# Optimization experiments

Hardware: AMD Instinct MI355X
Metric: run time of the kernel (lower is better)

## Reference

```python
import jax, jax.numpy as jnp
import numpy as np

N = 50000
E = 800000
NODE_F = 5
MAP_F = 32
EDGE_F = 4
HID = 64
RNN = 20
RNN_E = 8
LAT = 32
OUT = 4


def setup_inputs() -> dict:
    key = jax.random.key(0)
    ks = iter(jax.random.split(key, 40))
    def rn(shape, scale=0.1):
        return jax.random.normal(next(ks), shape, dtype=jnp.float32) * scale
    inp = {
        "x": rn((N, NODE_F), 1.0),
        "u": rn((N, MAP_F), 1.0),
        "edge_index": jax.random.randint(next(ks), (2, E), 0, N, dtype=jnp.int32),
        "edge_attr": rn((E, EDGE_F), 1.0),
        "h_node_h": rn((N, RNN), 1.0),
        "h_node_c": rn((N, RNN), 1.0),
        "h_edge_h": rn((N, RNN_E), 1.0),
        "h_edge_c": rn((N, RNN_E), 1.0),
        # node-history LSTM (input = node_features + map_encoding_size = 37)
        "W_ih_n": rn((4 * RNN, NODE_F + MAP_F)), "W_hh_n": rn((4 * RNN, RNN)),
        "b_ih_n": jnp.zeros((4 * RNN,), jnp.float32), "b_hh_n": jnp.zeros((4 * RNN,), jnp.float32),
        # edge-history LSTM (input = latent_edge_features)
        "W_ih_e": rn((4 * RNN_E, LAT)), "W_hh_e": rn((4 * RNN_E, RNN_E)),
        "b_ih_e": jnp.zeros((4 * RNN_E,), jnp.float32), "b_hh_e": jnp.zeros((4 * RNN_E,), jnp.float32),
        # message edge MLP: in = 2*37 + 4 = 78 -> 64 -> 32
        "We1": rn((2 * (NODE_F + MAP_F) + EDGE_F, HID)), "be1": jnp.zeros((HID,), jnp.float32),
        "We2": rn((HID, LAT)), "be2": jnp.zeros((LAT,), jnp.float32),
        # GN_out edge MLP: in = 2*(rnn_size + rnn_edge_size) + 4 = 60 -> 64 -> 32
        "Wo1": rn((2 * (RNN + RNN_E) + EDGE_F, HID)), "bo1": jnp.zeros((HID,), jnp.float32),
        "Wo2": rn((HID, LAT)), "bo2": jnp.zeros((LAT,), jnp.float32),
        # GN_out node MLP: in = (rnn_size + rnn_edge_size) + latent = 60 -> 64 -> 4
        "Wn1": rn((RNN + RNN_E + LAT, HID)), "bn1": jnp.zeros((HID,), jnp.float32),
        "Wn2": rn((HID, OUT)), "bn2": jnp.zeros((OUT,), jnp.float32),
    }
    return inp


def _lstm_step(xin, h, c, Wih, Whh, bih, bhh):
    # torch gate order: i, f, g, o
    g = xin @ Wih.T + h @ Whh.T + bih + bhh
    i, f, gg, o = jnp.split(g, 4, axis=-1)
    c_new = jax.nn.sigmoid(f) * c + jax.nn.sigmoid(i) * jnp.tanh(gg)
    h_new = jax.nn.sigmoid(o) * jnp.tanh(c_new)
    return h_new, c_new


def _segment_mean(vals, idx, n):
    s = jax.ops.segment_sum(vals, idx, num_segments=n)
    cnt = jax.ops.segment_sum(jnp.ones((vals.shape[0], 1), vals.dtype), idx, num_segments=n)
    return s / jnp.maximum(cnt, 1.0)


def _edge_mlp(src, dst, edge_attr, W1, b1, W2, b2):
    h = jnp.concatenate([src, dst, edge_attr], axis=-1)
    return jax.nn.relu(h @ W1 + b1) @ W2 + b2


def reference(x, u, edge_index, edge_attr, h_node_h, h_node_c, h_edge_h, h_edge_c,
              W_ih_n, W_hh_n, b_ih_n, b_hh_n, W_ih_e, W_hh_e, b_ih_e, b_hh_e,
              We1, be1, We2, be2, Wo1, bo1, Wo2, bo2, Wn1, bn1, Wn2, bn2):
    n = x.shape[0]
    xu = jnp.concatenate([x, u], axis=-1)  # [N, 37]
    # node history RNN step
    node_hist, node_c = _lstm_step(xu, h_node_h, h_node_c, W_ih_n, W_hh_n, b_ih_n, b_hh_n)
    # message GN: gather -> edge MLP
    row, col = edge_index[0], edge_index[1]
    messages = _edge_mlp(xu[row], xu[col], edge_attr, We1, be1, We2, be2)  # [E, 32]
    # edge history RNN: aggregate messages per receiving node, then LSTM step
    agg_msg = _segment_mean(messages, col, n)  # [N, 32]
    edge_hist, edge_c = _lstm_step(agg_msg, h_edge_h, h_edge_c, W_ih_e, W_hh_e, b_ih_e, b_hh_e)
    # output GN block
    full = jnp.concatenate([node_hist, edge_hist], axis=-1)  # [N, 28]
    e2 = _edge_mlp(full[row], full[col], edge_attr, Wo1, bo1, Wo2, bo2)  # [E, 32]
    agg2 = _segment_mean(e2, col, n)  # [N, 32]
    node_in = jnp.concatenate([full, agg2], axis=-1)  # [N, 60]
    out = jax.nn.relu(node_in @ Wn1 + bn1) @ Wn2 + bn2  # [N, 4]
    return (out, node_hist, node_c, edge_hist, edge_c)
```

## Files before the change

kernel.cpp:

```cpp
#include <hip/hip_runtime.h>
#include <math.h>

#define NN 50000
#define EE 800000
#define SBLK ((NN + 255) / 256)

typedef short bf16x8 __attribute__((ext_vector_type(8)));
typedef float f32x4 __attribute__((ext_vector_type(4)));
typedef unsigned short ushort_t;
#define MFMA16(a, b, c) __builtin_amdgcn_mfma_f32_16x16x32_bf16(a, b, c, 0, 0, 0)

__device__ __forceinline__ float sigmoidf_(float x) { return 1.0f / (1.0f + __expf(-x)); }

__device__ __forceinline__ unsigned short f2bf(float f) {
    unsigned u = __builtin_bit_cast(unsigned, f);
    u += 0x7FFFu + ((u >> 16) & 1u);
    return (unsigned short)(u >> 16);
}
__device__ __forceinline__ float bf2f(unsigned short v) {
    unsigned u = (unsigned)v << 16;
    return __builtin_bit_cast(float, u);
}
__device__ __forceinline__ unsigned pk2(float a, float b) {
    return ((unsigned)f2bf(b) << 16) | (unsigned)f2bf(a);
}

#define W1ST_A 104
#define W1ST_B 72
#define C1ST_  72
#define PW1A (64 * W1ST_A)
#define PW2A (32 * C1ST_)
#define PW1B (64 * W1ST_B)
#define PW2B (32 * C1ST_)

__global__ __launch_bounds__(256) void pack_w_k(
    const float* __restrict__ We1, const float* __restrict__ We2,
    const float* __restrict__ Wo1, const float* __restrict__ Wo2,
    ushort_t* __restrict__ pw)
{
    ushort_t* pw1a = pw;
    ushort_t* pw2a = pw1a + PW1A;
    ushort_t* pw1b = pw2a + PW2A;
    ushort_t* pw2b = pw1b + PW1B;
    int tid = threadIdx.x;

    for (int i = tid; i < PW1A; i += 256) {
        int n = i / W1ST_A, nk = i - n * W1ST_A;
        int kp = 0; bool z = false;
        if (nk < 37) kp = nk;
        else if (nk < 40) z = true;
        else if (nk < 77) kp = nk - 3;
        else if (nk < 80) z = true;
        else if (nk < 84) kp = nk - 6;
        else z = true;
        pw1a[i] = z ? (ushort_t)0 : f2bf(We1[kp * 64 + n]);
    }
    for (int i = tid; i < PW2A; i += 256) {
        int n = i / C1ST_, k = i - n * C1ST_;
        pw2a[i] = (k < 64) ? f2bf(We2[k * 32 + n]) : (ushort_t)0;
    }
    for (int i = tid; i < PW1B; i += 256) {
        int n = i / W1ST_B, nk = i - n * W1ST_B;
        int kp = 0; bool z = false;
        if (nk < 28) kp = nk;
        else if (nk < 32) z = true;
        else if (nk < 64) kp = nk - 4;
        else z = true;
        pw1b[i] = z ? (ushort_t)0 : f2bf(Wo1[kp * 64 + n]);
    }
    for (int i = tid; i < PW2B; i += 256) {
        int n = i / C1ST_, k = i - n * C1ST_;
        pw2b[i] = (k < 64) ? f2bf(Wo2[k * 32 + n]) : (ushort_t)0;
    }
}

__global__ __launch_bounds__(256) void node_lstm_k(
    const float* __restrict__ x, const float* __restrict__ u,
    const float* __restrict__ h0, const float* __restrict__ c0,
    const float* __restrict__ Wih, const float* __restrict__ Whh,
    const float* __restrict__ bih, const float* __restrict__ bhh,
    ushort_t* __restrict__ xu16, float* __restrict__ h_out, float* __restrict__ c_out)
{
    __shared__ float sWih[80 * 37];
    __shared__ float sWhh[80 * 20];
    __shared__ float sb[80];
    for (int i = threadIdx.x; i < 80 * 37; i += 256) sWih[i] = Wih[i];
    for (int i = threadIdx.x; i < 80 * 20; i += 256) sWhh[i] = Whh[i];
    if (threadIdx.x < 80) sb[threadIdx.x] = bih[threadIdx.x] + bhh[threadIdx.x];
    __syncthreads();
    int n = blockIdx.x * 256 + threadIdx.x;
    if (n >= NN) return;

    float xu[40];
#pragma unroll
    for (int k = 0; k < 5; k++) xu[k] = x[n * 5 + k];
#pragma unroll
    for (int k = 0; k < 32; k++) xu[5 + k] = u[n * 32 + k];
    xu[37] = 0.f; xu[38] = 0.f; xu[39] = 0.f;

    {
        unsigned w[20];
#pragma unroll
        for (int k = 0; k < 20; k++) w[k] = pk2(xu[2 * k], xu[2 * k + 1]);
        uint4* dst = (uint4*)(xu16 + (size_t)n * 40);
#pragma unroll
        for (int q = 0; q < 5; q++)
            dst[q] = make_uint4(w[q * 4], w[q * 4 + 1], w[q * 4 + 2], w[q * 4 + 3]);
    }

    float h[20];
#pragma unroll
    for (int k = 0; k < 20; k++) h[k] = h0[n * 20 + k];

#pragma unroll 1
    for (int r = 0; r < 20; r++) {
        float gi = sb[r], gf = sb[20 + r], gg = sb[40 + r], go = sb[60 + r];
#pragma unroll
        for (int k = 0; k < 37; k++) {
            float v = xu[k];
            gi = fmaf(v, sWih[r * 37 + k], gi);
            gf = fmaf(v, sWih[(20 + r) * 37 + k], gf);
            gg = fmaf(v, sWih[(40 + r) * 37 + k], gg);
            go = fmaf(v, sWih[(60 + r) * 37 + k], go);
        }
#pragma unroll
        for (int k = 0; k < 20; k++) {
            float v = h[k];
            gi = fmaf(v, sWhh[r * 20 + k], gi);
            gf = fmaf(v, sWhh[(20 + r) * 20 + k], gf);
            gg = fmaf(v, sWhh[(40 + r) * 20 + k], gg);
            go = fmaf(v, sWhh[(60 + r) * 20 + k], go);
        }
        float cr = c0[n * 20 + r];
        float cn = sigmoidf_(gf) * cr + sigmoidf_(gi) * tanhf(gg);
        float hn = sigmoidf_(go) * tanhf(cn);
        h_out[n * 20 + r] = hn;
        c_out[n * 20 + r] = cn;
    }
}

__global__ __launch_bounds__(256) void csr_count_k(const int* __restrict__ col,
                                                   int* __restrict__ count)
{
    int e = blockIdx.x * 256 + threadIdx.x;
    if (e < EE) atomicAdd(&count[col[e]], 1);
}

__global__ __launch_bounds__(256) void scan1_k(const int* __restrict__ count,
                                               int* __restrict__ bsum)
{
    __shared__ int red[256];
    int t = threadIdx.x;
    int i = blockIdx.x * 256 + t;
    red[t] = (i < NN) ? count[i] : 0;
    __syncthreads();
#pragma unroll
    for (int d = 128; d > 0; d >>= 1) {
        if (t < d) red[t] += red[t + d];
        __syncthreads();
    }
    if (t == 0) bsum[blockIdx.x] = red[0];
}

__global__ __launch_bounds__(256) void scan2_k(const int* __restrict__ bsum,
                                               int* __restrict__ bpre)
{
    __shared__ int s[256];
    int t = threadIdx.x;
    int v = (t < SBLK) ? bsum[t] : 0;
    s[t] = v;
    __syncthreads();
#pragma unroll
    for (int d = 1; d < 256; d <<= 1) {
        int w = (t >= d) ? s[t - d] : 0;
        __syncthreads();
        s[t] += w;
        __syncthreads();
    }
    if (t < SBLK) bpre[t] = s[t] - v;
}

__global__ __launch_bounds__(256) void scan3_k(const int* __restrict__ count,
                                               const int* __restrict__ bpre,
                                               int* __restrict__ offset,
                                               float* __restrict__ cntf)
{
    __shared__ int s[256];
    int t = threadIdx.x;
    int i = blockIdx.x * 256 + t;
    int v = (i < NN) ? count[i] : 0;
    s[t] = v;
    __syncthreads();
#pragma unroll
    for (int d = 1; d < 256; d <<= 1) {
        int w = (t >= d) ? s[t - d] : 0;
        __syncthreads();
        s[t] += w;
        __syncthreads();
    }
    if (i < NN) {
        offset[i] = bpre[blockIdx.x] + s[t] - v;
        cntf[i] = (float)v;
    }
}

__global__ __launch_bounds__(256) void csr_fill4_k(const int* __restrict__ row,
                                                   const int* __restrict__ col,
                                                   const float* __restrict__ eattr,
                                                   const int* __restrict__ offset,
                                                   int* __restrict__ cursor,
                                                   uint4* __restrict__ edat)
{
    int e = blockIdx.x * 256 + threadIdx.x;
    if (e >= EE) return;
    int c = col[e];
    int pos = atomicAdd(&cursor[c], 1);
    int slot = offset[c] + pos;
    float4 ev = *(const float4*)&eattr[(size_t)e * 4];
    edat[slot] = make_uint4((unsigned)row[e], (unsigned)c, pk2(ev.x, ev.y), pk2(ev.z, ev.w));
}

template <int F, int STRIDE, int INK>
__global__ __launch_bounds__(256, 5) void edge_mlp_fused_k(
    const ushort_t* __restrict__ feat,
    const uint4* __restrict__ edat,
    const int* __restrict__ offset, const int* __restrict__ count,
    const ushort_t* __restrict__ pw,
    const float* __restrict__ b1, const float* __restrict__ b2,
    float* __restrict__ agg)
{
    constexpr int S1 = INK / 32;
    constexpr int W1ST = INK + 8;
    constexpr int C1ST = C1ST_;
    constexpr int MST = 260;
    constexpr int ABYTES = (64 * W1ST + 32 * C1ST + 4 * 16 * C1ST) * 2;
    constexpr int BBYTES = 32 * MST * 2;
    constexpr int UBYTES = (ABYTES > BBYTES) ? ABYTES : BBYTES;
    constexpr int NU4 = (64 * W1ST + 32 * C1ST) / 8;

    __shared__ __align__(16) char ldsu[UBYTES];
    __shared__ int colLds[256];
    __shared__ unsigned char segStartA[256];
    __shared__ short segEndA[256];
    __shared__ int segCnt;

    ushort_t* sW1 = (ushort_t*)ldsu;
    ushort_t* sW2 = sW1 + 64 * W1ST;
    ushort_t* sC1 = sW2 + 32 * C1ST;
    ushort_t* msgT16 = (ushort_t*)ldsu;

    const int tid = threadIdx.x;
    const int B0 = blockIdx.x * 256;
    if (tid == 0) segCnt = 0;
    colLds[tid] = (int)edat[B0 + tid].y;

    {
        const uint4* src = (const uint4*)pw;
        uint4* dst = (uint4*)ldsu;
        for (int i = tid; i < NU4; i += 256) dst[i] = src[i];
    }
    __syncthreads();

    {
        bool isStart = (tid == 0) || (colLds[tid] != colLds[tid - 1]);
        if (isStart) {
            int node = colLds[tid];
            int off = offset[node], cn = count[node];
            int e = off + cn - B0; if (e > 256) e = 256;
            bool fullseg = (off >= B0) && (off + cn <= B0 + 256);
            int j = atomicAdd(&segCnt, 1);
            segStartA[j] = (unsigned char)tid;
            segEndA[j] = (short)(fullseg ? -e : e);
        }
    }

    const int wave = tid >> 6, lane = tid & 63;
    const int lr = lane & 15, jb = lane >> 4;
    const size_t slotBase = (size_t)B0 + (size_t)wave * 64;
    const float4* b1v = (const float4*)b1;
    ushort_t* myC1 = sC1 + wave * 16 * C1ST;
    const float bb2_0 = b2[lr], bb2_1 = b2[16 + lr];

    f32x4 acc2a[4][2];

#pragma unroll
    for (int q = 0; q < 4; q++) {
        bf16x8 xf[S1];
        {
            size_t slot = slotBase + (size_t)q * 16 + lr;
            uint4 ed = edat[slot];
            const ushort_t* xr = feat + (size_t)ed.x * STRIDE;
            const ushort_t* xc = feat + (size_t)ed.y * STRIDE;
            xf[0] = *(const bf16x8*)(xr + jb * 8);
            if (F == 37) {
                const ushort_t* p1 = (jb == 0) ? (xr + 32) : (xc + (jb - 1) * 8);
                xf[1] = *(const bf16x8*)p1;
                bf16x8 v;
                if (jb < 2) {
                    v = *(const bf16x8*)((jb == 0) ? (xc + 24) : (xc + 32));
                } else if (jb == 2) {
                    uint4 t = make_uint4(ed.z, ed.w, 0u, 0u);
                    v = __builtin_bit_cast(bf16x8, t);
                } else {
                    uint4 t = make_uint4(0u, 0u, 0u, 0u);
                    v = __builtin_bit_cast(bf16x8, t);
                }
                xf[2] = v;
            } else {
                if (jb < 3) {
                    xf[1] = *(const bf16x8*)(xc + jb * 8);
                } else {
                    uint2 lo = *(const uint2*)(xc + 24);
                    uint4 t = make_uint4(lo.x, lo.y, ed.z, ed.w);
                    xf[1] = __builtin_bit_cast(bf16x8, t);
                }
            }
        }

        f32x4 acc1[4];
#pragma unroll
        for (int mh = 0; mh < 4; mh++) {
            float4 bv = b1v[mh * 4 + jb];
            acc1[mh] = f32x4{bv.x, bv.y, bv.z, bv.w};
        }
#pragma unroll
        for (int s = 0; s < S1; s++) {
#pragma unroll
            for (int mh = 0; mh < 4; mh++) {
                bf16x8 wf = *(const bf16x8*)&sW1[(mh * 16 + lr) * W1ST + s * 32 + jb * 8];
                acc1[mh] = MFMA16(wf, xf[s], acc1[mh]);
            }
        }

#pragma unroll
        for (int mh = 0; mh < 4; mh++) {
            f32x4 a = acc1[mh];
            unsigned w0 = pk2(fmaxf(a[0], 0.f), fmaxf(a[1], 0.f));
            unsigned w1 = pk2(fmaxf(a[2], 0.f), fmaxf(a[3], 0.f));
            *(uint2*)&myC1[(jb * 4 + 0) * 0 + lr * C1ST + mh * 16 + jb * 4] = make_uint2(w0, w1);
        }

        acc2a[q][0] = f32x4{bb2_0, bb2_0, bb2_0, bb2_0};
        acc2a[q][1] = f32x4{bb2_1, bb2_1, bb2_1, bb2_1};
#pragma unroll
        for (int s2 = 0; s2 < 2; s2++) {
            bf16x8 w2f0 = *(const bf16x8*)&sW2[lr * C1ST + s2 * 32 + jb * 8];
            bf16x8 w2f1 = *(const bf16x8*)&sW2[(16 + lr) * C1ST + s2 * 32 + jb * 8];
            bf16x8 a2 = *(const bf16x8*)&myC1[lr * C1ST + s2 * 32 + jb * 8];
            acc2a[q][0] = MFMA16(a2, w2f0, acc2a[q][0]);
            acc2a[q][1] = MFMA16(a2, w2f1, acc2a[q][1]);
        }
    }

    __syncthreads();
#pragma unroll
    for (int q = 0; q < 4; q++) {
        int row = wave * 64 + q * 16 + jb * 4;
#pragma unroll
        for (int n = 0; n < 2; n++) {
            f32x4 a = acc2a[q][n];
            ushort_t* dst = &msgT16[(size_t)(n * 16 + lr) * MST + row];
            *(uint2*)dst = make_uint2(pk2(a[0], a[1]), pk2(a[2], a[3]));
        }
    }
    __syncthreads();

    {
        int f = lane & 31;
        int h = lane >> 5;
        const ushort_t* mrow = msgT16 + (size_t)f * MST;
        int nseg = segCnt;
        for (int j = wave; j < nseg; j += 4) {
            int s = segStartA[j];
            int ev = segEndA[j];
            bool fullseg = ev < 0;
            int e = fullseg ? -ev : ev;
            int node = colLds[s];
            float sum = 0.f;
            for (int i = s + h; i < e; i += 2) sum += bf2f(mrow[i]);
            sum += __shfl_xor(sum, 32);
            if (lane < 32) {
                float* dst = &agg[(size_t)node * 32 + f];
                if (fullseg) *dst = sum;
                else atomicAdd(dst, sum);
            }
        }
    }
}

__global__ __launch_bounds__(256) void edge_lstm_k(
    const float* __restrict__ agg, const float* __restrict__ cnt,
    const float* __restrict__ h0, const float* __restrict__ c0,
    const float* __restrict__ Wih, const float* __restrict__ Whh,
    const float* __restrict__ bih, const float* __restrict__ bhh,
    const float* __restrict__ node_h,
    float* __restrict__ h_out, float* __restrict__ c_out, ushort_t* __restrict__ full16)
{
    __shared__ float sWih[32 * 32];
    __shared__ float sWhh[32 * 8];
    __shared__ float sb[32];
    for (int i = threadIdx.x; i < 32 * 32; i += 256) sWih[i] = Wih[i];
    for (int i = threadIdx.x; i < 32 * 8; i += 256) sWhh[i] = Whh[i];
    if (threadIdx.x < 32) sb[threadIdx.x] = bih[threadIdx.x] + bhh[threadIdx.x];
    __syncthreads();
    int n = blockIdx.x * 256 + threadIdx.x;
    if (n >= NN) return;

    float inv = 1.0f / fmaxf(cnt[n], 1.0f);
    float msg[32];
#pragma unroll
    for (int k = 0; k < 32; k++) msg[k] = agg[(size_t)n * 32 + k] * inv;
    float h[8];
#pragma unroll
    for (int k = 0; k < 8; k++) h[k] = h0[n * 8 + k];

    float fl[32];
#pragma unroll
    for (int k = 0; k < 20; k++) fl[k] = node_h[n * 20 + k];
    fl[28] = 0.f; fl[29] = 0.f; fl[30] = 0.f; fl[31] = 0.f;

#pragma unroll
    for (int r = 0; r < 8; r++) {
        float gi = sb[r], gf = sb[8 + r], gg = sb[16 + r], go = sb[24 + r];
#pragma unroll
        for (int k = 0; k < 32; k++) {
            float v = msg[k];
            gi = fmaf(v, sWih[r * 32 + k], gi);
            gf = fmaf(v, sWih[(8 + r) * 32 + k], gf);
            gg = fmaf(v, sWih[(16 + r) * 32 + k], gg);
            go = fmaf(v, sWih[(24 + r) * 32 + k], go);
        }
#pragma unroll
        for (int k = 0; k < 8; k++) {
            float v = h[k];
            gi = fmaf(v, sWhh[r * 8 + k], gi);
            gf = fmaf(v, sWhh[(8 + r) * 8 + k], gf);
            gg = fmaf(v, sWhh[(16 + r) * 8 + k], gg);
            go = fmaf(v, sWhh[(24 + r) * 8 + k], go);
        }
        float cr = c0[n * 8 + r];
        float cn = sigmoidf_(gf) * cr + sigmoidf_(gi) * tanhf(gg);
        float hn = sigmoidf_(go) * tanhf(cn);
        h_out[n * 8 + r] = hn;
        c_out[n * 8 + r] = cn;
        fl[20 + r] = hn;
    }
    unsigned w[16];
#pragma unroll
    for (int k = 0; k < 16; k++) w[k] = pk2(fl[2 * k], fl[2 * k + 1]);
    uint4* dst = (uint4*)(full16 + (size_t)n * 32);
#pragma unroll
    for (int q = 0; q < 4; q++)
        dst[q] = make_uint4(w[q * 4], w[q * 4 + 1], w[q * 4 + 2], w[q * 4 + 3]);
}

__global__ __launch_bounds__(256) void node_out_k(
    const ushort_t* __restrict__ full16, const float* __restrict__ agg2, const float* __restrict__ cnt,
    const float* __restrict__ W1, const float* __restrict__ b1,
    const float* __restrict__ W2, const float* __restrict__ b2,
    float* __restrict__ out)
{
    __shared__ __align__(16) float sW1[60 * 64];
    __shared__ __align__(16) float sW2[64 * 4];
    __shared__ float sb1[64];
    __shared__ float sb2[4];
    for (int i = threadIdx.x; i < 60 * 64; i += 256) sW1[i] = W1[i];
    for (int i = threadIdx.x; i < 64 * 4; i += 256) sW2[i] = W2[i];
    if (threadIdx.x < 64) sb1[threadIdx.x] = b1[threadIdx.x];
    if (threadIdx.x < 4) sb2[threadIdx.x] = b2[threadIdx.x];
    __syncthreads();
    int n = blockIdx.x * 256 + threadIdx.x;
    if (n >= NN) return;

    float in[60];
    const ushort_t* fr = full16 + (size_t)n * 32;
#pragma unroll
    for (int k = 0; k < 28; k++) in[k] = bf2f(fr[k]);
    float inv = 1.0f / fmaxf(cnt[n], 1.0f);
#pragma unroll
    for (int k = 0; k < 32; k++) in[28 + k] = agg2[(size_t)n * 32 + k] * inv;

    float o[4] = {sb2[0], sb2[1], sb2[2], sb2[3]};
#pragma unroll 1
    for (int j = 0; j < 64; j += 4) {
        float s[4] = {sb1[j], sb1[j + 1], sb1[j + 2], sb1[j + 3]};
#pragma unroll
        for (int k = 0; k < 60; k++) {
            float4 w = *(const float4*)&sW1[k * 64 + j];
            s[0] = fmaf(in[k], w.x, s[0]);
            s[1] = fmaf(in[k], w.y, s[1]);
            s[2] = fmaf(in[k], w.z, s[2]);
            s[3] = fmaf(in[k], w.w, s[3]);
        }
#pragma unroll
        for (int jj = 0; jj < 4; jj++) {
            float sv = fmaxf(s[jj], 0.0f);
            float4 w = *(const float4*)&sW2[(j + jj) * 4];
            o[0] = fmaf(sv, w.x, o[0]);
            o[1] = fmaf(sv, w.y, o[1]);
            o[2] = fmaf(sv, w.z, o[2]);
            o[3] = fmaf(sv, w.w, o[3]);
        }
    }
#pragma unroll
    for (int m = 0; m < 4; m++) out[n * 4 + m] = o[m];
}

template <int F, int STRIDE, bool DO_CNT>
__global__ __launch_bounds__(256) void edge_mlp_atomic_k(
    const ushort_t* __restrict__ feat,
    const int* __restrict__ row, const int* __restrict__ col,
    const float* __restrict__ eattr,
    const float* __restrict__ W1, const float* __restrict__ b1,
    const float* __restrict__ W2, const float* __restrict__ b2,
    float* __restrict__ agg, float* __restrict__ cnt)
{
    constexpr int IN = 2 * F + 4;
    __shared__ __align__(16) float sW1[IN * 64];
    __shared__ __align__(16) float sW2[64 * 32];
    __shared__ float sb1[64];
    __shared__ float sb2[32];
    for (int i = threadIdx.x; i < IN * 64; i += 256) sW1[i] = W1[i];
    for (int i = threadIdx.x; i < 64 * 32; i += 256) sW2[i] = W2[i];
    if (threadIdx.x < 64) sb1[threadIdx.x] = b1[threadIdx.x];
    if (threadIdx.x < 32) sb2[threadIdx.x] = b2[threadIdx.x];
    __syncthreads();
    int e = blockIdx.x * 256 + threadIdx.x;
    if (e >= EE) return;

    int r = row[e], c = col[e];
    float h[IN];
#pragma unroll
    for (int k = 0; k < F; k++) h[k] = bf2f(feat[(size_t)r * STRIDE + k]);
#pragma unroll
    for (int k = 0; k < F; k++) h[F + k] = bf2f(feat[(size_t)c * STRIDE + k]);
    float4 ev = *(const float4*)&eattr[(size_t)e * 4];
    h[2 * F] = ev.x; h[2 * F + 1] = ev.y; h[2 * F + 2] = ev.z; h[2 * F + 3] = ev.w;

    float out[32];
#pragma unroll
    for (int m = 0; m < 32; m++) out[m] = sb2[m];
#pragma unroll 1
    for (int j = 0; j < 64; j += 4) {
        float s[4] = {sb1[j], sb1[j + 1], sb1[j + 2], sb1[j + 3]};
#pragma unroll
        for (int k = 0; k < IN; k++) {
            float4 w = *(const float4*)&sW1[k * 64 + j];
            s[0] = fmaf(h[k], w.x, s[0]);
            s[1] = fmaf(h[k], w.y, s[1]);
            s[2] = fmaf(h[k], w.z, s[2]);
            s[3] = fmaf(h[k], w.w, s[3]);
        }
        s[0] = fmaxf(s[0], 0.f); s[1] = fmaxf(s[1], 0.f);
        s[2] = fmaxf(s[2], 0.f); s[3] = fmaxf(s[3], 0.f);
#pragma unroll
        for (int jj = 0; jj < 4; jj++) {
#pragma unroll
            for (int m = 0; m < 32; m += 4) {
                float4 w = *(const float4*)&sW2[(j + jj) * 32 + m];
                out[m]     = fmaf(s[jj], w.x, out[m]);
                out[m + 1] = fmaf(s[jj], w.y, out[m + 1]);
                out[m + 2] = fmaf(s[jj], w.z, out[m + 2]);
                out[m + 3] = fmaf(s[jj], w.w, out[m + 3]);
            }
        }
    }
    float* dst = &agg[(size_t)c * 32];
#pragma unroll
    for (int m = 0; m < 32; m++) atomicAdd(&dst[m], out[m]);
    if (DO_CNT) atomicAdd(&cnt[c], 1.0f);
}

extern "C" void kernel_launch(void* const* d_in, const int* in_sizes, int n_in,
                              void* d_out, int out_size, void* d_ws, size_t ws_size,
                              hipStream_t stream) {
    (void)in_sizes; (void)n_in; (void)out_size;
    const float* x      = (const float*)d_in[0];
    const float* u      = (const float*)d_in[1];
    const int*   ei     = (const int*)d_in[2];
    const float* eattr  = (const float*)d_in[3];
    const float* hn_h   = (const float*)d_in[4];
    const float* hn_c   = (const float*)d_in[5];
    const float* he_h   = (const float*)d_in[6];
    const float* he_c   = (const float*)d_in[7];
    const float* Wih_n  = (const float*)d_in[8];
    const float* Whh_n  = (const float*)d_in[9];
    const float* bih_n  = (const float*)d_in[10];
    const float* bhh_n  = (const float*)d_in[11];
    const float* Wih_e  = (const float*)d_in[12];
    const float* Whh_e  = (const float*)d_in[13];
    const float* bih_e  = (const float*)d_in[14];
    const float* bhh_e  = (const float*)d_in[15];
    const float* We1    = (const float*)d_in[16];
    const float* be1    = (const float*)d_in[17];
    const float* We2    = (const float*)d_in[18];
    const float* be2    = (const float*)d_in[19];
    const float* Wo1    = (const float*)d_in[20];
    const float* bo1    = (const float*)d_in[21];
    const float* Wo2    = (const float*)d_in[22];
    const float* bo2    = (const float*)d_in[23];
    const float* Wn1    = (const float*)d_in[24];
    const float* bn1    = (const float*)d_in[25];
    const float* Wn2    = (const float*)d_in[26];
    const float* bn2    = (const float*)d_in[27];

    const int* row = ei;
    const int* col = ei + EE;

    float* out = (float*)d_out;
    float* out_y   = out;
    float* node_h  = out + (size_t)NN * 4;
    float* node_c  = out + (size_t)NN * 24;
    float* edge_h  = out + (size_t)NN * 44;
    float* edge_c  = out + (size_t)NN * 52;

    int nb_n = (NN + 255) / 256;
    int nb_e = (EE + 255) / 256;

    ushort_t* xu16   = (ushort_t*)d_ws;
    ushort_t* full16 = xu16 + (size_t)NN * 40;
    float* agg  = (float*)(full16 + (size_t)NN * 32);
    float* cntf = agg + (size_t)NN * 32;
    float* agg2 = cntf + NN;
    int* count  = (int*)(agg2 + (size_t)NN * 32);
    int* cursor = count + NN;
    int* offset = cursor + NN;
    int* bsum   = offset + NN;
    int* bpre   = bsum + SBLK;
    size_t pw_off = ((size_t)((char*)(bpre + SBLK) - (char*)d_ws) + 15) & ~(size_t)15;
    ushort_t* pw = (ushort_t*)((char*)d_ws + pw_off);
    size_t edat_off = ((pw_off + (size_t)(PW1A + PW2A + PW1B + PW2B) * 2) + 15) & ~(size_t)15;
    uint4* edat = (uint4*)((char*)d_ws + edat_off);
    size_t needed = edat_off + (size_t)EE * 16;

    if (ws_size >= needed) {
        hipMemsetAsync(agg, 0, (size_t)NN * (32 + 1 + 32 + 1 + 1) * sizeof(float), stream);

        pack_w_k<<<1, 256, 0, stream>>>(We1, We2, Wo1, Wo2, pw);
        node_lstm_k<<<nb_n, 256, 0, stream>>>(x, u, hn_h, hn_c, Wih_n, Whh_n, bih_n, bhh_n,
                                              xu16, node_h, node_c);
        csr_count_k<<<nb_e, 256, 0, stream>>>(col, count);
        scan1_k<<<SBLK, 256, 0, stream>>>(count, bsum);
        scan2_k<<<1, 256, 0, stream>>>(bsum, bpre);
        scan3_k<<<SBLK, 256, 0, stream>>>(count, bpre, offset, cntf);
        csr_fill4_k<<<nb_e, 256, 0, stream>>>(row, col, eattr, offset, cursor, edat);

        edge_mlp_fused_k<37, 40, 96><<<EE / 256, 256, 0, stream>>>(
            xu16, edat, offset, count, pw, be1, be2, agg);
        edge_lstm_k<<<nb_n, 256, 0, stream>>>(agg, cntf, he_h, he_c, Wih_e, Whh_e, bih_e, bhh_e,
                                              node_h, edge_h, edge_c, full16);
        edge_mlp_fused_k<28, 32, 64><<<EE / 256, 256, 0, stream>>>(
            full16, edat, offset, count, pw + PW1A + PW2A, bo1, bo2, agg2);
        node_out_k<<<nb_n, 256, 0, stream>>>(full16, agg2, cntf, Wn1, bn1, Wn2, bn2, out_y);
    } else {
        hipMemsetAsync(agg, 0, (size_t)NN * (32 + 1 + 32) * sizeof(float), stream);
        node_lstm_k<<<nb_n, 256, 0, stream>>>(x, u, hn_h, hn_c, Wih_n, Whh_n, bih_n, bhh_n,
                                              xu16, node_h, node_c);
        edge_mlp_atomic_k<37, 40, true><<<nb_e, 256, 0, stream>>>(xu16, row, col, eattr,
                                                                  We1, be1, We2, be2, agg, cntf);
        edge_lstm_k<<<nb_n, 256, 0, stream>>>(agg, cntf, he_h, he_c, Wih_e, Whh_e, bih_e, bhh_e,
                                              node_h, edge_h, edge_c, full16);
        edge_mlp_atomic_k<28, 32, false><<<nb_e, 256, 0, stream>>>(full16, row, col, eattr,
                                                                   Wo1, bo1, Wo2, bo2, agg2, nullptr);
        node_out_k<<<nb_n, 256, 0, stream>>>(full16, agg2, cntf, Wn1, bn1, Wn2, bn2, out_y);
    }
}
```

Measured before the change: 261.6 us.

## Merge small setup kernels and software-pipeline edge gathers in fused edge MLP

Fuses the edge-count atomic pass with the node LSTM in one launch using block-index ranges, and folds the weight packing into the first scan kernel as an extra block. This removes two kernel launches and lets independent work share the GPU. Inside the fused edge MLP, the gather of edge features is now double-buffered so the next quarter's loads are issued before the current quarter's MFMAs. The launch-bounds occupancy hint drops from 5 to 4 blocks to make room for the extra registers the prefetch needs.

```diff
diff --git a/kernel.cpp b/kernel.cpp
--- a/kernel.cpp
+++ b/kernel.cpp
@@ -4,6 +4,7 @@
 #define NN 50000
 #define EE 800000
 #define SBLK ((NN + 255) / 256)
+#define NBE ((EE + 255) / 256)
 
 typedef short bf16x8 __attribute__((ext_vector_type(8)));
 typedef float f32x4 __attribute__((ext_vector_type(4)));
@@ -33,48 +34,8 @@
 #define PW1B (64 * W1ST_B)
 #define PW2B (32 * C1ST_)
 
-__global__ __launch_bounds__(256) void pack_w_k(
-    const float* __restrict__ We1, const float* __restrict__ We2,
-    const float* __restrict__ Wo1, const float* __restrict__ Wo2,
-    ushort_t* __restrict__ pw)
-{
-    ushort_t* pw1a = pw;
-    ushort_t* pw2a = pw1a + PW1A;
-    ushort_t* pw1b = pw2a + PW2A;
-    ushort_t* pw2b = pw1b + PW1B;
-    int tid = threadIdx.x;
-
-    for (int i = tid; i < PW1A; i += 256) {
-        int n = i / W1ST_A, nk = i - n * W1ST_A;
-        int kp = 0; bool z = false;
-        if (nk < 37) kp = nk;
-        else if (nk < 40) z = true;
-        else if (nk < 77) kp = nk - 3;
-        else if (nk < 80) z = true;
-        else if (nk < 84) kp = nk - 6;
-        else z = true;
-        pw1a[i] = z ? (ushort_t)0 : f2bf(We1[kp * 64 + n]);
-    }
-    for (int i = tid; i < PW2A; i += 256) {
-        int n = i / C1ST_, k = i - n * C1ST_;
-        pw2a[i] = (k < 64) ? f2bf(We2[k * 32 + n]) : (ushort_t)0;
-    }
-    for (int i = tid; i < PW1B; i += 256) {
-        int n = i / W1ST_B, nk = i - n * W1ST_B;
-        int kp = 0; bool z = false;
-        if (nk < 28) kp = nk;
-        else if (nk < 32) z = true;
-        else if (nk < 64) kp = nk - 4;
-        else z = true;
-        pw1b[i] = z ? (ushort_t)0 : f2bf(Wo1[kp * 64 + n]);
-    }
-    for (int i = tid; i < PW2B; i += 256) {
-        int n = i / C1ST_, k = i - n * C1ST_;
-        pw2b[i] = (k < 64) ? f2bf(Wo2[k * 32 + n]) : (ushort_t)0;
-    }
-}
-
-__global__ __launch_bounds__(256) void node_lstm_k(
+__global__ __launch_bounds__(256) void count_lstm_k(
+    const int* __restrict__ col, int* __restrict__ count,
     const float* __restrict__ x, const float* __restrict__ u,
     const float* __restrict__ h0, const float* __restrict__ c0,
     const float* __restrict__ Wih, const float* __restrict__ Whh,
@@ -84,11 +45,18 @@
     __shared__ float sWih[80 * 37];
     __shared__ float sWhh[80 * 20];
     __shared__ float sb[80];
+
+    if (blockIdx.x < NBE) {
+        int e = blockIdx.x * 256 + threadIdx.x;
+        if (e < EE) atomicAdd(&count[col[e]], 1);
+        return;
+    }
+
     for (int i = threadIdx.x; i < 80 * 37; i += 256) sWih[i] = Wih[i];
     for (int i = threadIdx.x; i < 80 * 20; i += 256) sWhh[i] = Whh[i];
     if (threadIdx.x < 80) sb[threadIdx.x] = bih[threadIdx.x] + bhh[threadIdx.x];
     __syncthreads();
-    int n = blockIdx.x * 256 + threadIdx.x;
+    int n = (blockIdx.x - NBE) * 256 + threadIdx.x;
     if (n >= NN) return;
 
     float xu[40];
@@ -139,18 +107,49 @@
     }
 }
 
-__global__ __launch_bounds__(256) void csr_count_k(const int* __restrict__ col,
-                                                   int* __restrict__ count)
-{
-    int e = blockIdx.x * 256 + threadIdx.x;
-    if (e < EE) atomicAdd(&count[col[e]], 1);
-}
-
-__global__ __launch_bounds__(256) void scan1_k(const int* __restrict__ count,
-                                               int* __restrict__ bsum)
+__global__ __launch_bounds__(256) void scan1p_k(
+    const int* __restrict__ count, int* __restrict__ bsum,
+    const float* __restrict__ We1, const float* __restrict__ We2,
+    const float* __restrict__ Wo1, const float* __restrict__ Wo2,
+    ushort_t* __restrict__ pw)
 {
     __shared__ int red[256];
     int t = threadIdx.x;
+    if (blockIdx.x == SBLK) {
+        ushort_t* pw1a = pw;
+        ushort_t* pw2a = pw1a + PW1A;
+        ushort_t* pw1b = pw2a + PW2A;
+        ushort_t* pw2b = pw1b + PW1B;
+        for (int i = t; i < PW1A; i += 256) {
+            int n = i / W1ST_A, nk = i - n * W1ST_A;
+            int kp = 0; bool z = false;
+            if (nk < 37) kp = nk;
+            else if (nk < 40) z = true;
+            else if (nk < 77) kp = nk - 3;
+            else if (nk < 80) z = true;
+            else if (nk < 84) kp = nk - 6;
+            else z = true;
+            pw1a[i] = z ? (ushort_t)0 : f2bf(We1[kp * 64 + n]);
+        }
+        for (int i = t; i < PW2A; i += 256) {
+            int n = i / C1ST_, k = i - n * C1ST_;
+            pw2a[i] = (k < 64) ? f2bf(We2[k * 32 + n]) : (ushort_t)0;
+        }
+        for (int i = t; i < PW1B; i += 256) {
+            int n = i / W1ST_B, nk = i - n * W1ST_B;
+            int kp = 0; bool z = false;
+            if (nk < 28) kp = nk;
+            else if (nk < 32) z = true;
+            else if (nk < 64) kp = nk - 4;
+            else z = true;
+            pw1b[i] = z ? (ushort_t)0 : f2bf(Wo1[kp * 64 + n]);
+        }
+        for (int i = t; i < PW2B; i += 256) {
+            int n = i / C1ST_, k = i - n * C1ST_;
+            pw2b[i] = (k < 64) ? f2bf(Wo2[k * 32 + n]) : (ushort_t)0;
+        }
+        return;
+    }
     int i = blockIdx.x * 256 + t;
     red[t] = (i < NN) ? count[i] : 0;
     __syncthreads();
@@ -220,8 +219,43 @@
     edat[slot] = make_uint4((unsigned)row[e], (unsigned)c, pk2(ev.x, ev.y), pk2(ev.z, ev.w));
 }
 
+template <int F, int STRIDE, int S1>
+__device__ __forceinline__ void gather_frag(
+    const ushort_t* __restrict__ feat, const uint4* __restrict__ edat,
+    size_t slotBase, int q, int lr, int jb, bf16x8* xf)
+{
+    size_t slot = slotBase + (size_t)q * 16 + lr;
+    uint4 ed = edat[slot];
+    const ushort_t* xr = feat + (size_t)ed.x * STRIDE;
+    const ushort_t* xc = feat + (size_t)ed.y * STRIDE;
+    xf[0] = *(const bf16x8*)(xr + jb * 8);
+    if (F == 37) {
+        const ushort_t* p1 = (jb == 0) ? (xr + 32) : (xc + (jb - 1) * 8);
+        xf[1] = *(const bf16x8*)p1;
+        bf16x8 v;
+        if (jb < 2) {
+            v = *(const bf16x8*)((jb == 0) ? (xc + 24) : (xc + 32));
+        } else if (jb == 2) {
+            uint4 t = make_uint4(ed.z, ed.w, 0u, 0u);
+            v = __builtin_bit_cast(bf16x8, t);
+        } else {
+            uint4 t = make_uint4(0u, 0u, 0u, 0u);
+            v = __builtin_bit_cast(bf16x8, t);
+        }
+        xf[2] = v;
+    } else {
+        if (jb < 3) {
+            xf[1] = *(const bf16x8*)(xc + jb * 8);
+        } else {
+            uint2 lo = *(const uint2*)(xc + 24);
+            uint4 t = make_uint4(lo.x, lo.y, ed.z, ed.w);
+            xf[1] = __builtin_bit_cast(bf16x8, t);
+        }
+    }
+}
+
 template <int F, int STRIDE, int INK>
-__global__ __launch_bounds__(256, 5) void edge_mlp_fused_k(
+__global__ __launch_bounds__(256, 4) void edge_mlp_fused_k(
     const ushort_t* __restrict__ feat,
     const uint4* __restrict__ edat,
     const int* __restrict__ offset, const int* __restrict__ count,
@@ -281,42 +315,7 @@
     ushort_t* myC1 = sC1 + wave * 16 * C1ST;
     const float bb2_0 = b2[lr], bb2_1 = b2[16 + lr];
 
-    f32x4 acc2a[4][2];
-
-#pragma unroll
-    for (int q = 0; q < 4; q++) {
-        bf16x8 xf[S1];
-        {
-            size_t slot = slotBase + (size_t)q * 16 + lr;
-            uint4 ed = edat[slot];
-            const ushort_t* xr = feat + (size_t)ed.x * STRIDE;
-            const ushort_t* xc = feat + (size_t)ed.y * STRIDE;
-            xf[0] = *(const bf16x8*)(xr + jb * 8);
-            if (F == 37) {
-                const ushort_t* p1 = (jb == 0) ? (xr + 32) : (xc + (jb - 1) * 8);
-                xf[1] = *(const bf16x8*)p1;
-                bf16x8 v;
-                if (jb < 2) {
-                    v = *(const bf16x8*)((jb == 0) ? (xc + 24) : (xc + 32));
-                } else if (jb == 2) {
-                    uint4 t = make_uint4(ed.z, ed.w, 0u, 0u);
-                    v = __builtin_bit_cast(bf16x8, t);
-                } else {
-                    uint4 t = make_uint4(0u, 0u, 0u, 0u);
-                    v = __builtin_bit_cast(bf16x8, t);
-                }
-                xf[2] = v;
-            } else {
-                if (jb < 3) {
-                    xf[1] = *(const bf16x8*)(xc + jb * 8);
-                } else {
-                    uint2 lo = *(const uint2*)(xc + 24);
-                    uint4 t = make_uint4(lo.x, lo.y, ed.z, ed.w);
-                    xf[1] = __builtin_bit_cast(bf16x8, t);
-                }
-            }
-        }
-
+    auto compute = [&](const bf16x8* xf, f32x4& o0, f32x4& o1) {
         f32x4 acc1[4];
 #pragma unroll
         for (int mh = 0; mh < 4; mh++) {
@@ -331,38 +330,48 @@
                 acc1[mh] = MFMA16(wf, xf[s], acc1[mh]);
             }
         }
-
 #pragma unroll
         for (int mh = 0; mh < 4; mh++) {
             f32x4 a = acc1[mh];
             unsigned w0 = pk2(fmaxf(a[0], 0.f), fmaxf(a[1], 0.f));
             unsigned w1 = pk2(fmaxf(a[2], 0.f), fmaxf(a[3], 0.f));
-            *(uint2*)&myC1[(jb * 4 + 0) * 0 + lr * C1ST + mh * 16 + jb * 4] = make_uint2(w0, w1);
-        }
-
-        acc2a[q][0] = f32x4{bb2_0, bb2_0, bb2_0, bb2_0};
-        acc2a[q][1] = f32x4{bb2_1, bb2_1, bb2_1, bb2_1};
+            *(uint2*)&myC1[lr * C1ST + mh * 16 + jb * 4] = make_uint2(w0, w1);
+        }
+        o0 = f32x4{bb2_0, bb2_0, bb2_0, bb2_0};
+        o1 = f32x4{bb2_1, bb2_1, bb2_1, bb2_1};
 #pragma unroll
         for (int s2 = 0; s2 < 2; s2++) {
             bf16x8 w2f0 = *(const bf16x8*)&sW2[lr * C1ST + s2 * 32 + jb * 8];
             bf16x8 w2f1 = *(const bf16x8*)&sW2[(16 + lr) * C1ST + s2 * 32 + jb * 8];
             bf16x8 a2 = *(const bf16x8*)&myC1[lr * C1ST + s2 * 32 + jb * 8];
-            acc2a[q][0] = MFMA16(a2, w2f0, acc2a[q][0]);
-            acc2a[q][1] = MFMA16(a2, w2f1, acc2a[q][1]);
-        }
-    }
-
-    __syncthreads();
-#pragma unroll
-    for (int q = 0; q < 4; q++) {
-        int row = wave * 64 + q * 16 + jb * 4;
-#pragma unroll
-        for (int n = 0; n < 2; n++) {
-            f32x4 a = acc2a[q][n];
-            ushort_t* dst = &msgT16[(size_t)(n * 16 + lr) * MST + row];
-            *(uint2*)dst = make_uint2(pk2(a[0], a[1]), pk2(a[2], a[3]));
-        }
-    }
+            o0 = MFMA16(a2, w2f0, o0);
+            o1 = MFMA16(a2, w2f1, o1);
+        }
+    };
+
+    f32x4 a00, a01, a10, a11, a20, a21, a30, a31;
+    bf16x8 xfA[S1], xfB[S1];
+    gather_frag<F, STRIDE, S1>(feat, edat, slotBase, 0, lr, jb, xfA);
+    gather_frag<F, STRIDE, S1>(feat, edat, slotBase, 1, lr, jb, xfB);
+    compute(xfA, a00, a01);
+    gather_frag<F, STRIDE, S1>(feat, edat, slotBase, 2, lr, jb, xfA);
+    compute(xfB, a10, a11);
+    gather_frag<F, STRIDE, S1>(feat, edat, slotBase, 3, lr, jb, xfB);
+    compute(xfA, a20, a21);
+    compute(xfB, a30, a31);
+
+    __syncthreads();
+#define DUMPQ(qq, A0, A1) { \
+        int row = wave * 64 + (qq) * 16 + jb * 4; \
+        { f32x4 a = (A0); ushort_t* dst = &msgT16[(size_t)lr * MST + row]; \
+          *(uint2*)dst = make_uint2(pk2(a[0], a[1]), pk2(a[2], a[3])); } \
+        { f32x4 a = (A1); ushort_t* dst = &msgT16[(size_t)(16 + lr) * MST + row]; \
+          *(uint2*)dst = make_uint2(pk2(a[0], a[1]), pk2(a[2], a[3])); } }
+    DUMPQ(0, a00, a01)
+    DUMPQ(1, a10, a11)
+    DUMPQ(2, a20, a21)
+    DUMPQ(3, a30, a31)
+#undef DUMPQ
     __syncthreads();
 
     {
@@ -504,6 +513,68 @@
     }
 #pragma unroll
     for (int m = 0; m < 4; m++) out[n * 4 + m] = o[m];
+}
+
+__global__ __launch_bounds__(256) void node_lstm_k(
+    const float* __restrict__ x, const float* __restrict__ u,
+    const float* __restrict__ h0, const float* __restrict__ c0,
+    const float* __restrict__ Wih, const float* __restrict__ Whh,
+    const float* __restrict__ bih, const float* __restrict__ bhh,
+    ushort_t* __restrict__ xu16, float* __restrict__ h_out, float* __restrict__ c_out)
+{
+    __shared__ float sWih[80 * 37];
+    __shared__ float sWhh[80 * 20];
+    __shared__ float sb[80];
+    for (int i = threadIdx.x; i < 80 * 37; i += 256) sWih[i] = Wih[i];
+    for (int i = threadIdx.x; i < 80 * 20; i += 256) sWhh[i] = Whh[i];
+    if (threadIdx.x < 80) sb[threadIdx.x] = bih[threadIdx.x] + bhh[threadIdx.x];
+    __syncthreads();
+    int n = blockIdx.x * 256 + threadIdx.x;
+    if (n >= NN) return;
+
+    float xu[40];
+#pragma unroll
+    for (int k = 0; k < 5; k++) xu[k] = x[n * 5 + k];
+#pragma unroll
+    for (int k = 0; k < 32; k++) xu[5 + k] = u[n * 32 + k];
+    xu[37] = 0.f; xu[38] = 0.f; xu[39] = 0.f;
+    {
+        unsigned w[20];
+#pragma unroll
+        for (int k = 0; k < 20; k++) w[k] = pk2(xu[2 * k], xu[2 * k + 1]);
+        uint4* dst = (uint4*)(xu16 + (size_t)n * 40);
+#pragma unroll
+        for (int q = 0; q < 5; q++)
+            dst[q] = make_uint4(w[q * 4], w[q * 4 + 1], w[q * 4 + 2], w[q * 4 + 3]);
+    }
+    float h[20];
+#pragma unroll
+    for (int k = 0; k < 20; k++) h[k] = h0[n * 20 + k];
+#pragma unroll 1
+    for (int r = 0; r < 20; r++) {
+        float gi = sb[r], gf = sb[20 + r], gg = sb[40 + r], go = sb[60 + r];
+#pragma unroll
+        for (int k = 0; k < 37; k++) {
+            float v = xu[k];
+            gi = fmaf(v, sWih[r * 37 + k], gi);
+            gf = fmaf(v, sWih[(20 + r) * 37 + k], gf);
+            gg = fmaf(v, sWih[(40 + r) * 37 + k], gg);
+            go = fmaf(v, sWih[(60 + r) * 37 + k], go);
+        }
+#pragma unroll
+        for (int k = 0; k < 20; k++) {
+            float v = h[k];
+            gi = fmaf(v, sWhh[r * 20 + k], gi);
+            gf = fmaf(v, sWhh[(20 + r) * 20 + k], gf);
+            gg = fmaf(v, sWhh[(40 + r) * 20 + k], gg);
+            go = fmaf(v, sWhh[(60 + r) * 20 + k], go);
+        }
+        float cr = c0[n * 20 + r];
+        float cn = sigmoidf_(gf) * cr + sigmoidf_(gi) * tanhf(gg);
+        float hn = sigmoidf_(go) * tanhf(cn);
+        h_out[n * 20 + r] = hn;
+        c_out[n * 20 + r] = cn;
+    }
 }
 
 template <int F, int STRIDE, bool DO_CNT>
@@ -615,7 +686,7 @@
     float* edge_c  = out + (size_t)NN * 52;
 
     int nb_n = (NN + 255) / 256;
-    int nb_e = (EE + 255) / 256;
+    int nb_e = NBE;
 
     ushort_t* xu16   = (ushort_t*)d_ws;
     ushort_t* full16 = xu16 + (size_t)NN * 40;
@@ -636,11 +707,10 @@
     if (ws_size >= needed) {
         hipMemsetAsync(agg, 0, (size_t)NN * (32 + 1 + 32 + 1 + 1) * sizeof(float), stream);
 
-        pack_w_k<<<1, 256, 0, stream>>>(We1, We2, Wo1, Wo2, pw);
-        node_lstm_k<<<nb_n, 256, 0, stream>>>(x, u, hn_h, hn_c, Wih_n, Whh_n, bih_n, bhh_n,
-                                              xu16, node_h, node_c);
-        csr_count_k<<<nb_e, 256, 0, stream>>>(col, count);
-        scan1_k<<<SBLK, 256, 0, stream>>>(count, bsum);
+        count_lstm_k<<<nb_e + nb_n, 256, 0, stream>>>(
+            col, count, x, u, hn_h, hn_c, Wih_n, Whh_n, bih_n, bhh_n,
+            xu16, node_h, node_c);
+        scan1p_k<<<SBLK + 1, 256, 0, stream>>>(count, bsum, We1, We2, Wo1, Wo2, pw);
         scan2_k<<<1, 256, 0, stream>>>(bsum, bpre);
         scan3_k<<<SBLK, 256, 0, stream>>>(count, bpre, offset, cntf);
         csr_fill4_k<<<nb_e, 256, 0, stream>>>(row, col, eattr, offset, cursor, edat);
```

Result: slower. 269.2 us (+2.9%).
